# Kernel optimization log

Hardware: AMD Instinct MI355X
Metric: run time of the kernel (lower is better)

## Reference

```python
import jax, jax.numpy as jnp
import numpy as np

B, T, D, K = 16, 3000, 512, 3
N_TOK = 448          # static max token count (targets are <= 448)
N_MAX = N_TOK + 1    # scatter bins incl. overflow bin, matches torch n_max
LN_EPS = 1e-5


def setup_inputs() -> dict:
    key = jax.random.key(0)
    k0, k1, k2, k3, k4 = jax.random.split(key, 5)
    encoder_1d = jax.random.normal(k0, (B, T, D), jnp.float32)
    # depthwise conv kernel [D, 1, K] (torch Conv1d groups=D, no bias)
    conv_w = jax.random.normal(k1, (D, 1, K), jnp.float32) * (1.0 / np.sqrt(K))
    ln_gamma = jnp.ones((D,), jnp.float32)
    ln_beta = jnp.zeros((D,), jnp.float32)
    proj_w = jax.random.normal(k2, (D,), jnp.float32) * (1.0 / np.sqrt(D))
    alpha_init = min(2048.0 / 3000.0, 0.99)
    proj_b = jnp.float32(np.log(alpha_init / (1.0 - alpha_init)))
    input_lengths = jax.random.randint(k3, (B,), T // 2, T + 1).astype(jnp.int32)
    target_lengths = jax.random.randint(k4, (B,), 300, N_TOK + 1).astype(jnp.int32)
    return {"encoder_1d": encoder_1d, "conv_w": conv_w, "ln_gamma": ln_gamma,
            "ln_beta": ln_beta, "proj_w": proj_w, "proj_b": proj_b,
            "input_lengths": input_lengths, "target_lengths": target_lengths}


def _cif(encoder_1d, conv_w, ln_gamma, ln_beta, proj_w, proj_b,
         input_lengths, target_lengths):
    dt = encoder_1d.dtype
    # ---- weight predictor: depthwise conv + LN + linear + sigmoid ----
    x = jnp.transpose(encoder_1d, (0, 2, 1))                      # [B, D, T]
    x = jax.lax.conv_general_dilated(
        x, conv_w, window_strides=(1,), padding=[(K // 2, K // 2)],
        dimension_numbers=("NCH", "OIH", "NCH"), feature_group_count=D)
    x = jnp.transpose(x, (0, 2, 1))                               # [B, T, D]
    mu = jnp.mean(x, axis=-1, keepdims=True)
    var = jnp.mean(jnp.square(x - mu), axis=-1, keepdims=True)
    x = (x - mu) * jax.lax.rsqrt(var + LN_EPS) * ln_gamma + ln_beta
    alpha = jax.nn.sigmoid(jnp.einsum("btd,d->bt", x, proj_w) + proj_b)  # [B, T]
    # ---- padding mask ----
    valid = jnp.arange(T)[None, :] < input_lengths[:, None]
    alpha = jnp.where(valid, alpha, jnp.zeros((), dt))
    # ---- quantity loss ----
    tgt = target_lengths.astype(dt)
    sum_alpha = jnp.sum(alpha, axis=1)
    qty_loss = jnp.mean(jnp.abs(sum_alpha - tgt))
    # ---- training-mode rescale so cumsum ends exactly at target ----
    alpha_cif = alpha * (tgt / jnp.maximum(sum_alpha, 1e-8))[:, None]
    # ---- CIF integration: cumsum + two scatter-adds ----
    cum = jnp.cumsum(alpha_cif, axis=1)                           # [B, T]
    cum_prev = jnp.pad(cum[:, :-1], ((0, 0), (1, 0)))
    k_lo = jnp.floor(cum_prev).astype(jnp.int32)
    k_hi = jnp.floor(cum).astype(jnp.int32)
    boundary = (k_lo + 1).astype(dt)
    w_lo = jnp.maximum(jnp.minimum(cum, boundary) - cum_prev, 0.0)
    w_hi = jnp.maximum(cum - boundary, 0.0)
    bidx = jnp.arange(B)[:, None]                                 # [B, 1] -> bcast [B, T]
    out = jnp.zeros((B, N_MAX, D), dt)
    out = out.at[bidx, jnp.clip(k_lo, 0, N_MAX - 1)].add(encoder_1d * w_lo[..., None])
    out = out.at[bidx, jnp.clip(k_hi, 0, N_MAX - 1)].add(encoder_1d * w_hi[..., None])
    return out[:, :N_TOK], alpha, qty_loss


def reference(encoder_1d, conv_w, ln_gamma, ln_beta, proj_w, proj_b,
              input_lengths, target_lengths):
    return _cif(encoder_1d, conv_w, ln_gamma, ln_beta, proj_w, proj_b,
                input_lengths, target_lengths)
```

## Files before the change

kernel.cpp:

```cpp
#include <hip/hip_runtime.h>
#include <math.h>

#define B_ 16
#define T_ 3000
#define D_ 512
#define NTOK 448
#define LN_EPS 1e-5f

#define WS_DIFF 16
#define WS_CUM  64
#define WS_STG  (64 + B_ * T_)

struct F8 { float v[8]; };

__device__ inline F8 load8(const float* __restrict__ p) {
    F8 r;
    float4 a = *(const float4*)p;
    float4 b = *(const float4*)(p + 4);
    r.v[0]=a.x; r.v[1]=a.y; r.v[2]=a.z; r.v[3]=a.w;
    r.v[4]=b.x; r.v[5]=b.y; r.v[6]=b.z; r.v[7]=b.w;
    return r;
}

__global__ __launch_bounds__(512) void k_const(
    const float* __restrict__ projw, const float* __restrict__ gamma,
    const float* __restrict__ beta, const float* __restrict__ projb,
    float* __restrict__ ws)
{
    __shared__ float r0[512], r1[512];
    int d = threadIdx.x;
    r0[d] = projw[d] * beta[d];
    r1[d] = projw[d] * gamma[d];
    __syncthreads();
    for (int off = 256; off > 0; off >>= 1) {
        if (d < off) { r0[d] += r0[d + off]; r1[d] += r1[d + off]; }
        __syncthreads();
    }
    if (d == 0) { ws[0] = r0[0] + projb[0]; ws[1] = r1[0]; }
}

__global__ __launch_bounds__(256) void k_alpha(
    const float* __restrict__ enc, const float* __restrict__ convw,
    const float* __restrict__ gamma, const float* __restrict__ projw,
    const int* __restrict__ ilen, const float* __restrict__ cst,
    float* __restrict__ alpha_out)
{
    const int NB = 188;
    int wave = threadIdx.x >> 6;
    int lane = threadIdx.x & 63;
    int b  = blockIdx.x / NB;
    int tb = blockIdx.x % NB;
    int t0 = tb * 16 + wave * 4;
    int d0 = lane * 8;
    if (t0 >= T_) return;

    const float* rowp = enc + ((size_t)b * T_ + t0) * D_ + d0;

    F8 r[6];
#pragma unroll
    for (int i = 0; i < 6; ++i) {
        int t = t0 - 1 + i;
        if (t >= 0 && t < T_) r[i] = load8(rowp + (ptrdiff_t)(i - 1) * D_);
        else { for (int j = 0; j < 8; ++j) r[i].v[j] = 0.f; }
    }

    float w24[24];
    const float4* wp = (const float4*)(convw + (size_t)d0 * 3);
#pragma unroll
    for (int i = 0; i < 6; ++i) {
        float4 q = wp[i];
        w24[4*i+0]=q.x; w24[4*i+1]=q.y; w24[4*i+2]=q.z; w24[4*i+3]=q.w;
    }
    F8 pw = load8(projw + d0);
    F8 gm = load8(gamma + d0);
    float pg[8];
#pragma unroll
    for (int j = 0; j < 8; ++j) pg[j] = pw.v[j] * gm.v[j];

    float s1[4], s2[4], sp[4];
#pragma unroll
    for (int q = 0; q < 4; ++q) { s1[q]=0.f; s2[q]=0.f; sp[q]=0.f; }

#pragma unroll
    for (int q = 0; q < 4; ++q) {
#pragma unroll
        for (int j = 0; j < 8; ++j) {
            float y = r[q].v[j]*w24[3*j] + r[q+1].v[j]*w24[3*j+1] + r[q+2].v[j]*w24[3*j+2];
            s1[q] += y; s2[q] += y*y; sp[q] += pg[j]*y;
        }
    }
#pragma unroll
    for (int off = 1; off < 64; off <<= 1) {
#pragma unroll
        for (int q = 0; q < 4; ++q) {
            s1[q] += __shfl_xor(s1[q], off);
            s2[q] += __shfl_xor(s2[q], off);
            sp[q] += __shfl_xor(sp[q], off);
        }
    }
    if (lane == 0) {
        int il = ilen[b];
        float c0 = cst[0], c1 = cst[1];
#pragma unroll
        for (int q = 0; q < 4; ++q) {
            int t = t0 + q;
            if (t >= T_) break;
            float mu  = s1[q] * (1.0f / D_);
            float var = s2[q] * (1.0f / D_) - mu * mu;
            float rsig = rsqrtf(var + LN_EPS);
            float logit = rsig * (sp[q] - mu * c1) + c0;
            float a = 1.0f / (1.0f + expf(-logit));
            if (t >= il) a = 0.0f;
            alpha_out[b * T_ + t] = a;
        }
    }
}

__global__ __launch_bounds__(512) void k_prep(
    const float* __restrict__ alpha, const int* __restrict__ tlen,
    float* __restrict__ ws)
{
    __shared__ float sc[T_];
    __shared__ float red[512];
    __shared__ float part[8];

    int b = blockIdx.x;
    int tid = threadIdx.x;
    int wave = tid >> 6;
    int lane = tid & 63;

    float* cumg = ws + WS_CUM + (size_t)b * T_;
    int*   stg  = (int*)(ws + WS_STG) + b * 450;

    float s = 0.f;
    for (int t = tid; t < T_; t += 512) { float a = alpha[b * T_ + t]; sc[t] = a; s += a; }
    red[tid] = s;
    __syncthreads();
    for (int off = 256; off > 0; off >>= 1) {
        if (tid < off) red[tid] += red[tid + off];
        __syncthreads();
    }
    float sum = red[0];
    float tgt = (float)tlen[b];
    float scale = tgt / fmaxf(sum, 1e-8f);
    if (tid == 0) ws[WS_DIFF + b] = fabsf(sum - tgt);
    __syncthreads();

    float run = 0.f;
    for (int base = 0; base < T_; base += 512) {
        int t = base + tid;
        float v = (t < T_) ? sc[t] * scale : 0.f;
#pragma unroll
        for (int off = 1; off < 64; off <<= 1) {
            float n = __shfl_up(v, off);
            if (lane >= off) v += n;
        }
        if (lane == 63) part[wave] = v;
        __syncthreads();
        float prefix = run;
        for (int w = 0; w < 8; ++w) {
            float pv = part[w];
            if (w < wave) prefix += pv;
            run += pv;
        }
        v += prefix;
        if (t < T_) { sc[t] = v; cumg[t] = v; }
        __syncthreads();
    }

    for (int k = tid; k < 450; k += 512) {
        float vk = (float)k;
        int lo = 0, hi = T_;
        while (lo < hi) {
            int mid = (lo + hi) >> 1;
            if (sc[mid] < vk) lo = mid + 1; else hi = mid;
        }
        stg[k] = lo;
    }
}

__global__ __launch_bounds__(64) void k_qty(
    const float* __restrict__ ws, float* __restrict__ qty)
{
    if (threadIdx.x == 0) {
        float q = 0.f;
        for (int i = 0; i < B_; ++i) q += ws[WS_DIFF + i];
        *qty = q * (1.0f / B_);
    }
}

__global__ __launch_bounds__(256) void k_gather(
    const float* __restrict__ enc, const float* __restrict__ ws,
    const int* __restrict__ ilen, float* __restrict__ out)
{
    const int NBLK = NTOK / 8;
    int b  = blockIdx.x / NBLK;
    int kg = blockIdx.x % NBLK;
    int wave = threadIdx.x >> 6;
    int lane = threadIdx.x & 63;
    int k0 = kg * 8 + wave * 2;

    const float* cb  = ws + WS_CUM + (size_t)b * T_;
    const int*   stg = (const int*)(ws + WS_STG) + b * 450;

    int il = ilen[b];
    int a = stg[k0];
    int e = stg[k0 + 2] + 1;
    if (e > il) e = il;

    int d0 = lane * 8;
    const float* encb = enc + (size_t)b * T_ * D_ + d0;

    float4 a0a = {0,0,0,0}, a0b = {0,0,0,0};
    float4 a1a = {0,0,0,0}, a1b = {0,0,0,0};

    float fk0 = (float)k0, fk1 = (float)(k0 + 1);

    for (int base = a; base < e; base += 32) {
        int n = e - base; if (n > 32) n = 32;
        float cl = 0.0f;
        int t = base - 1 + lane;
        if (lane <= n && t >= 0) cl = cb[t];

        for (int j = 0; j < n; ++j) {
            float cp = __shfl(cl, j);
            float c  = __shfl(cl, j + 1);
            float fklo = floorf(cp);
            float fkhi = floorf(c);
            float bnd  = fklo + 1.0f;
            float wlo  = fmaxf(fminf(c, bnd) - cp, 0.0f);
            float whi  = fmaxf(c - bnd, 0.0f);
            float w0 = (fklo == fk0 ? wlo : 0.0f) + (fkhi == fk0 ? whi : 0.0f);
            float w1 = (fklo == fk1 ? wlo : 0.0f) + (fkhi == fk1 ? whi : 0.0f);
            if (w0 != 0.0f || w1 != 0.0f) {
                const float* rp = encb + (size_t)(base + j) * D_;
                float4 ea = *(const float4*)rp;
                float4 eb = *(const float4*)(rp + 4);
                a0a.x += ea.x*w0; a0a.y += ea.y*w0; a0a.z += ea.z*w0; a0a.w += ea.w*w0;
                a0b.x += eb.x*w0; a0b.y += eb.y*w0; a0b.z += eb.z*w0; a0b.w += eb.w*w0;
                a1a.x += ea.x*w1; a1a.y += ea.y*w1; a1a.z += ea.z*w1; a1a.w += ea.w*w1;
                a1b.x += eb.x*w1; a1b.y += eb.y*w1; a1b.z += eb.z*w1; a1b.w += eb.w*w1;
            }
        }
    }

    float* op = out + ((size_t)b * NTOK + k0) * D_ + d0;
    *(float4*)op        = a0a;
    *(float4*)(op + 4)  = a0b;
    *(float4*)(op + D_)     = a1a;
    *(float4*)(op + D_ + 4) = a1b;
}

extern "C" void kernel_launch(void* const* d_in, const int* in_sizes, int n_in,
                              void* d_out, int out_size, void* d_ws, size_t ws_size,
                              hipStream_t stream) {
    const float* enc   = (const float*)d_in[0];
    const float* convw = (const float*)d_in[1];
    const float* gamma = (const float*)d_in[2];
    const float* beta  = (const float*)d_in[3];
    const float* projw = (const float*)d_in[4];
    const float* projb = (const float*)d_in[5];
    const int*   ilen  = (const int*)d_in[6];
    const int*   tlen  = (const int*)d_in[7];

    float* out_f     = (float*)d_out;
    float* alpha_out = out_f + (size_t)B_ * NTOK * D_;
    float* qty_out   = alpha_out + (size_t)B_ * T_;

    float* ws = (float*)d_ws;

    hipLaunchKernelGGL(k_const, dim3(1), dim3(512), 0, stream,
                       projw, gamma, beta, projb, ws);
    hipLaunchKernelGGL(k_alpha, dim3(B_ * 188), dim3(256), 0, stream,
                       enc, convw, gamma, projw, ilen, ws, alpha_out);
    hipLaunchKernelGGL(k_prep, dim3(B_), dim3(512), 0, stream,
                       alpha_out, tlen, ws);
    hipLaunchKernelGGL(k_qty, dim3(1), dim3(64), 0, stream,
                       ws, qty_out);
    hipLaunchKernelGGL(k_gather, dim3(B_ * (NTOK / 8)), dim3(256), 0, stream,
                       enc, ws, ilen, out_f);
}
```

Baseline: 55.96 us.

## Fuse constant and qty kernels, single-pass scan, one token per wave in gather

Removes the k_const kernel by having each k_alpha wave reduce the projection constants itself, and folds the qty-loss reduction into an extra block of the gather kernel. This cuts the launch count from five to three. k_prep now runs one prefix scan over raw alpha and scales the result by tgt/sum afterwards, which drops the separate reduction pass. The gather assigns one token per wave with precomputed per-lane weights broadcast by shuffle and no branch, so there are more blocks and more parallelism. The cost is redundant constant reductions in every wave and unconditional row loads in the gather.

```diff
diff --git a/kernel.cpp b/kernel.cpp
--- a/kernel.cpp
+++ b/kernel.cpp
@@ -22,28 +22,11 @@
     return r;
 }
 
-__global__ __launch_bounds__(512) void k_const(
-    const float* __restrict__ projw, const float* __restrict__ gamma,
-    const float* __restrict__ beta, const float* __restrict__ projb,
-    float* __restrict__ ws)
-{
-    __shared__ float r0[512], r1[512];
-    int d = threadIdx.x;
-    r0[d] = projw[d] * beta[d];
-    r1[d] = projw[d] * gamma[d];
-    __syncthreads();
-    for (int off = 256; off > 0; off >>= 1) {
-        if (d < off) { r0[d] += r0[d + off]; r1[d] += r1[d + off]; }
-        __syncthreads();
-    }
-    if (d == 0) { ws[0] = r0[0] + projb[0]; ws[1] = r1[0]; }
-}
-
 __global__ __launch_bounds__(256) void k_alpha(
     const float* __restrict__ enc, const float* __restrict__ convw,
-    const float* __restrict__ gamma, const float* __restrict__ projw,
-    const int* __restrict__ ilen, const float* __restrict__ cst,
-    float* __restrict__ alpha_out)
+    const float* __restrict__ gamma, const float* __restrict__ beta,
+    const float* __restrict__ projw, const float* __restrict__ projb,
+    const int* __restrict__ ilen, float* __restrict__ alpha_out)
 {
     const int NB = 188;
     int wave = threadIdx.x >> 6;
@@ -73,9 +56,15 @@
     }
     F8 pw = load8(projw + d0);
     F8 gm = load8(gamma + d0);
+    F8 bt = load8(beta + d0);
     float pg[8];
-#pragma unroll
-    for (int j = 0; j < 8; ++j) pg[j] = pw.v[j] * gm.v[j];
+    float c0p = 0.f, c1p = 0.f;
+#pragma unroll
+    for (int j = 0; j < 8; ++j) {
+        pg[j] = pw.v[j] * gm.v[j];
+        c0p += pw.v[j] * bt.v[j];
+        c1p += pg[j];
+    }
 
     float s1[4], s2[4], sp[4];
 #pragma unroll
@@ -97,10 +86,13 @@
             s2[q] += __shfl_xor(s2[q], off);
             sp[q] += __shfl_xor(sp[q], off);
         }
+        c0p += __shfl_xor(c0p, off);
+        c1p += __shfl_xor(c1p, off);
     }
     if (lane == 0) {
         int il = ilen[b];
-        float c0 = cst[0], c1 = cst[1];
+        float c0 = c0p + projb[0];
+        float c1 = c1p;
 #pragma unroll
         for (int q = 0; q < 4; ++q) {
             int t = t0 + q;
@@ -121,7 +113,6 @@
     float* __restrict__ ws)
 {
     __shared__ float sc[T_];
-    __shared__ float red[512];
     __shared__ float part[8];
 
     int b = blockIdx.x;
@@ -132,24 +123,10 @@
     float* cumg = ws + WS_CUM + (size_t)b * T_;
     int*   stg  = (int*)(ws + WS_STG) + b * 450;
 
-    float s = 0.f;
-    for (int t = tid; t < T_; t += 512) { float a = alpha[b * T_ + t]; sc[t] = a; s += a; }
-    red[tid] = s;
-    __syncthreads();
-    for (int off = 256; off > 0; off >>= 1) {
-        if (tid < off) red[tid] += red[tid + off];
-        __syncthreads();
-    }
-    float sum = red[0];
-    float tgt = (float)tlen[b];
-    float scale = tgt / fmaxf(sum, 1e-8f);
-    if (tid == 0) ws[WS_DIFF + b] = fabsf(sum - tgt);
-    __syncthreads();
-
     float run = 0.f;
     for (int base = 0; base < T_; base += 512) {
         int t = base + tid;
-        float v = (t < T_) ? sc[t] * scale : 0.f;
+        float v = (t < T_) ? alpha[b * T_ + t] : 0.f;
 #pragma unroll
         for (int off = 1; off < 64; off <<= 1) {
             float n = __shfl_up(v, off);
@@ -164,9 +141,21 @@
             run += pv;
         }
         v += prefix;
-        if (t < T_) { sc[t] = v; cumg[t] = v; }
+        if (t < T_) sc[t] = v;
         __syncthreads();
     }
+
+    float sum = run;
+    float tgt = (float)tlen[b];
+    float scale = tgt / fmaxf(sum, 1e-8f);
+    if (tid == 0) ws[WS_DIFF + b] = fabsf(sum - tgt);
+
+    for (int t = tid; t < T_; t += 512) {
+        float cv = sc[t] * scale;
+        sc[t] = cv;
+        cumg[t] = cv;
+    }
+    __syncthreads();
 
     for (int k = tid; k < 450; k += 512) {
         float vk = (float)k;
@@ -179,76 +168,71 @@
     }
 }
 
-__global__ __launch_bounds__(64) void k_qty(
-    const float* __restrict__ ws, float* __restrict__ qty)
-{
-    if (threadIdx.x == 0) {
-        float q = 0.f;
-        for (int i = 0; i < B_; ++i) q += ws[WS_DIFF + i];
-        *qty = q * (1.0f / B_);
-    }
-}
-
 __global__ __launch_bounds__(256) void k_gather(
     const float* __restrict__ enc, const float* __restrict__ ws,
-    const int* __restrict__ ilen, float* __restrict__ out)
+    const int* __restrict__ ilen, float* __restrict__ out,
+    float* __restrict__ qty)
 {
-    const int NBLK = NTOK / 8;
-    int b  = blockIdx.x / NBLK;
-    int kg = blockIdx.x % NBLK;
+    int bid = blockIdx.x;
+    if (bid == B_ * 112) {
+        int lane = threadIdx.x;
+        if (lane < 64) {
+            float v = (lane < B_) ? ws[WS_DIFF + lane] : 0.f;
+#pragma unroll
+            for (int off = 1; off < 16; off <<= 1) v += __shfl_xor(v, off);
+            if (lane == 0) *qty = v * (1.0f / B_);
+        }
+        return;
+    }
+
+    const int NBLK = NTOK / 4;
+    int b  = bid / NBLK;
+    int kg = bid % NBLK;
     int wave = threadIdx.x >> 6;
     int lane = threadIdx.x & 63;
-    int k0 = kg * 8 + wave * 2;
+    int k = kg * 4 + wave;
 
     const float* cb  = ws + WS_CUM + (size_t)b * T_;
     const int*   stg = (const int*)(ws + WS_STG) + b * 450;
 
     int il = ilen[b];
-    int a = stg[k0];
-    int e = stg[k0 + 2] + 1;
+    int a = stg[k];
+    int e = stg[k + 1] + 1;
     if (e > il) e = il;
 
     int d0 = lane * 8;
     const float* encb = enc + (size_t)b * T_ * D_ + d0;
 
-    float4 a0a = {0,0,0,0}, a0b = {0,0,0,0};
-    float4 a1a = {0,0,0,0}, a1b = {0,0,0,0};
-
-    float fk0 = (float)k0, fk1 = (float)(k0 + 1);
-
-    for (int base = a; base < e; base += 32) {
-        int n = e - base; if (n > 32) n = 32;
+    float4 aa = {0,0,0,0}, ab = {0,0,0,0};
+    float fk = (float)k;
+
+    for (int base = a; base < e; base += 63) {
+        int n = e - base; if (n > 63) n = 63;
         float cl = 0.0f;
         int t = base - 1 + lane;
         if (lane <= n && t >= 0) cl = cb[t];
-
+        float cn = __shfl_down(cl, 1);
+        float fklo = floorf(cl);
+        float bnd  = fklo + 1.0f;
+        float wlo  = fmaxf(fminf(cn, bnd) - cl, 0.0f);
+        float whi  = fmaxf(cn - bnd, 0.0f);
+        float wl = (fklo == fk ? wlo : 0.0f) + (floorf(cn) == fk ? whi : 0.0f);
+        if (lane >= n) wl = 0.0f;
+
+#pragma unroll 4
         for (int j = 0; j < n; ++j) {
-            float cp = __shfl(cl, j);
-            float c  = __shfl(cl, j + 1);
-            float fklo = floorf(cp);
-            float fkhi = floorf(c);
-            float bnd  = fklo + 1.0f;
-            float wlo  = fmaxf(fminf(c, bnd) - cp, 0.0f);
-            float whi  = fmaxf(c - bnd, 0.0f);
-            float w0 = (fklo == fk0 ? wlo : 0.0f) + (fkhi == fk0 ? whi : 0.0f);
-            float w1 = (fklo == fk1 ? wlo : 0.0f) + (fkhi == fk1 ? whi : 0.0f);
-            if (w0 != 0.0f || w1 != 0.0f) {
-                const float* rp = encb + (size_t)(base + j) * D_;
-                float4 ea = *(const float4*)rp;
-                float4 eb = *(const float4*)(rp + 4);
-                a0a.x += ea.x*w0; a0a.y += ea.y*w0; a0a.z += ea.z*w0; a0a.w += ea.w*w0;
-                a0b.x += eb.x*w0; a0b.y += eb.y*w0; a0b.z += eb.z*w0; a0b.w += eb.w*w0;
-                a1a.x += ea.x*w1; a1a.y += ea.y*w1; a1a.z += ea.z*w1; a1a.w += ea.w*w1;
-                a1b.x += eb.x*w1; a1b.y += eb.y*w1; a1b.z += eb.z*w1; a1b.w += eb.w*w1;
-            }
-        }
-    }
-
-    float* op = out + ((size_t)b * NTOK + k0) * D_ + d0;
-    *(float4*)op        = a0a;
-    *(float4*)(op + 4)  = a0b;
-    *(float4*)(op + D_)     = a1a;
-    *(float4*)(op + D_ + 4) = a1b;
+            float w = __shfl(wl, j);
+            const float* rp = encb + (size_t)(base + j) * D_;
+            float4 ea = *(const float4*)rp;
+            float4 eb = *(const float4*)(rp + 4);
+            aa.x += ea.x*w; aa.y += ea.y*w; aa.z += ea.z*w; aa.w += ea.w*w;
+            ab.x += eb.x*w; ab.y += eb.y*w; ab.z += eb.z*w; ab.w += eb.w*w;
+        }
+    }
+
+    float* op = out + ((size_t)b * NTOK + k) * D_ + d0;
+    *(float4*)op       = aa;
+    *(float4*)(op + 4) = ab;
 }
 
 extern "C" void kernel_launch(void* const* d_in, const int* in_sizes, int n_in,
@@ -269,14 +253,10 @@
 
     float* ws = (float*)d_ws;
 
-    hipLaunchKernelGGL(k_const, dim3(1), dim3(512), 0, stream,
-                       projw, gamma, beta, projb, ws);
     hipLaunchKernelGGL(k_alpha, dim3(B_ * 188), dim3(256), 0, stream,
-                       enc, convw, gamma, projw, ilen, ws, alpha_out);
+                       enc, convw, gamma, beta, projw, projb, ilen, alpha_out);
     hipLaunchKernelGGL(k_prep, dim3(B_), dim3(512), 0, stream,
                        alpha_out, tlen, ws);
-    hipLaunchKernelGGL(k_qty, dim3(1), dim3(64), 0, stream,
-                       ws, qty_out);
-    hipLaunchKernelGGL(k_gather, dim3(B_ * (NTOK / 8)), dim3(256), 0, stream,
-                       enc, ws, ilen, out_f);
-}
+    hipLaunchKernelGGL(k_gather, dim3(B_ * 112 + 1), dim3(256), 0, stream,
+                       enc, ws, ilen, out_f, qty_out);
+}
```

Result: faster. 51.36 us (-8.2%).
